# Kernel optimization log

Hardware: AMD Instinct MI355X
Metric: run time of the kernel (lower is better)

The kernel has to match this reference:

```python
import jax, jax.numpy as jnp
import numpy as np

N = 100000      # nodes
E = 3200000     # edges
F_IN = 128      # input feature dim
H = 256         # hidden dim
K = 30          # num_cluster
REG = 0.01      # regularizer coefficient


def _uniform(key, shape, fan_in):
    s = 1.0 / np.sqrt(fan_in)
    return jax.random.uniform(key, shape, jnp.float32, -s, s)


def setup_inputs() -> dict:
    key = jax.random.key(0)
    ks = jax.random.split(key, 11)
    x = jax.random.normal(ks[0], (N, F_IN), jnp.float32)
    edge_index = jax.random.randint(ks[1], (2, E), 0, N, jnp.int32)
    edge_attr = jax.random.uniform(ks[2], (E,), jnp.float32)
    return dict(
        x=x, edge_index=edge_index, edge_attr=edge_attr,
        W_conv1=_uniform(ks[3], (F_IN, H), F_IN), b_conv1=jnp.zeros((H,), jnp.float32),
        W_lin1=_uniform(ks[4], (F_IN, H), F_IN),  b_lin1=_uniform(ks[5], (H,), F_IN),
        W_conv2=_uniform(ks[6], (H, K), H),       b_conv2=jnp.zeros((K,), jnp.float32),
        W_lin2=_uniform(ks[7], (H, K), H),        b_lin2=_uniform(ks[8], (K,), H),
    )


def gcn_conv(x, W, b, row, col, w):
    """PyG GCNConv: symmetric-normalized, edge-weighted aggregation with self-loops (weight 1)."""
    n = x.shape[0]
    deg = jax.ops.segment_sum(w, col, num_segments=n) + 1.0  # self-loop weight 1
    dis = jax.lax.rsqrt(deg)                                  # deg > 0 always (self-loop)
    norm = dis[row] * w * dis[col]                            # [E]
    h = x @ W                                                 # [n, out]
    agg = jax.ops.segment_sum(norm[:, None] * h[row], col, num_segments=n)
    agg = agg + (dis * dis)[:, None] * h                      # self-loop contribution
    return agg + b


def reference(x, edge_index, edge_attr,
              W_conv1, b_conv1, W_lin1, b_lin1,
              W_conv2, b_conv2, W_lin2, b_lin2):
    row, col = edge_index[0], edge_index[1]
    # dropout is identity in eval mode
    h = jax.nn.relu(gcn_conv(x, W_conv1, b_conv1, row, col, edge_attr) + x @ W_lin1 + b_lin1)
    out = gcn_conv(h, W_conv2, b_conv2, row, col, edge_attr) + h @ W_lin2 + b_lin2
    FX = jnp.clip(jax.nn.softmax(out, axis=-1), 1e-9, 1.0 - 1e-9)  # [N, K]

    # modularity loss
    m = jnp.sum(edge_attr)
    degree = jax.ops.segment_sum(edge_attr, row, num_segments=x.shape[0])  # [N]
    connectivity = jnp.sum(edge_attr * jnp.sum(FX[row, :-1] * FX[col, :-1], axis=-1))
    s = jnp.sum(FX * degree[:, None], axis=0)[:-1]
    avg_connectivity = jnp.dot(s, s) / (2.0 * m)
    modularity = -(connectivity - avg_connectivity) / (2.0 * m)

    # collapse regularizer
    reg = (jnp.sqrt(jnp.sum(jnp.sum(FX, axis=0) ** 2) + 1e-9)
           * (FX.shape[-1] ** 0.5) / FX.shape[0] - 1.0)
    return FX, modularity + REG * reg
```

## Files before the change

kernel.cpp:

```cpp
#include <hip/hip_runtime.h>
#include <hip/hip_bf16.h>
#include <math.h>

#define N_NODES 100000
#define N_EDGES 3200000
#define F_IN 128
#define HID 256
#define KCL 30
#define NCOPY 8

typedef unsigned int uint;
typedef unsigned short ushort;
typedef unsigned char uchar;
typedef __attribute__((ext_vector_type(8))) short bf16x8;
typedef __attribute__((ext_vector_type(4))) float f32x4;
typedef __attribute__((ext_vector_type(2))) float f32x2;

static __device__ __forceinline__ float bf2f(ushort u) {
  return __uint_as_float(((uint)u) << 16);
}
static __device__ __forceinline__ ushort f2bf(float f) {
  uint u = __float_as_uint(f);
  uint r = (u + 0x7FFF + ((u >> 16) & 1)) >> 16;
  return (ushort)r;
}

static __device__ __forceinline__ uchar f2fp8(float f) {
#if __has_builtin(__builtin_amdgcn_cvt_pk_fp8_f32)
  return (uchar)(__builtin_amdgcn_cvt_pk_fp8_f32(f, f, 0, false) & 0xFF);
#else
  uint u = __float_as_uint(f);
  uint s = (u >> 24) & 0x80u;
  float a = fabsf(f);
  if (a >= 448.f) return (uchar)(s | 0x7E);
  if (a < 0.015625f) {
    int q = (int)rintf(a * 512.f);
    return (uchar)(s | (q > 8 ? 8 : q));
  }
  int e = ((int)((u >> 23) & 0xFF)) - 127;
  float step = __uint_as_float((uint)(127 + e - 3) << 23);
  int q = (int)rintf(a / step);
  if (q == 16) { e += 1; q = 8; }
  return (uchar)(s | ((e + 7) << 3) | (q - 8));
#endif
}
static __device__ __forceinline__ float fp82f_sw(uchar b) {
  uint s = ((uint)(b & 0x80u)) << 24;
  uint em = b & 0x7Fu;
  float mag;
  if ((em >> 3) == 0) mag = (float)em * 0.001953125f;
  else mag = __uint_as_float((((em >> 3) + 120) << 23) | ((em & 7u) << 20));
  return __uint_as_float(s | __float_as_uint(mag));
}
static __device__ __forceinline__ void fp8x4_dec(uint u, float* o) {
#if __has_builtin(__builtin_amdgcn_cvt_pk_f32_fp8)
  f32x2 lo = __builtin_amdgcn_cvt_pk_f32_fp8((int)u, false);
  f32x2 hi = __builtin_amdgcn_cvt_pk_f32_fp8((int)u, true);
  o[0] = lo.x; o[1] = lo.y; o[2] = hi.x; o[3] = hi.y;
#else
  o[0] = fp82f_sw(u & 0xFF); o[1] = fp82f_sw((u >> 8) & 0xFF);
  o[2] = fp82f_sw((u >> 16) & 0xFF); o[3] = fp82f_sw((u >> 24) & 0xFF);
#endif
}
static __device__ __forceinline__ float fp81_dec(uchar b) {
#if __has_builtin(__builtin_amdgcn_cvt_pk_f32_fp8)
  f32x2 lo = __builtin_amdgcn_cvt_pk_f32_fp8((int)(uint)b, false);
  return lo.x;
#else
  return fp82f_sw(b);
#endif
}
static __device__ __forceinline__ void dec29(uint4 lo, uint4 hi, float* f) {
  fp8x4_dec(lo.x, f + 0);  fp8x4_dec(lo.y, f + 4);
  fp8x4_dec(lo.z, f + 8);  fp8x4_dec(lo.w, f + 12);
  fp8x4_dec(hi.x, f + 16); fp8x4_dec(hi.y, f + 20);
  fp8x4_dec(hi.z, f + 24);
  f[28] = fp81_dec((uchar)(hi.w & 0xFF));
}


__global__ __launch_bounds__(256) void k_cnt8(const int* __restrict__ ei,
                                              int* __restrict__ cnt8) {
  int e0 = (blockIdx.x * 256 + threadIdx.x) * 4;
  int g = blockIdx.x & (NCOPY - 1);
  int4 cc = *(const int4*)(ei + N_EDGES + e0);
  int* tab = cnt8 + (size_t)g * N_NODES;
  atomicAdd(tab + cc.x, 1);
  atomicAdd(tab + cc.y, 1);
  atomicAdd(tab + cc.z, 1);
  atomicAdd(tab + cc.w, 1);
}

__global__ __launch_bounds__(1024) void k_scanA(const int* __restrict__ cnt8,
                                                int* __restrict__ off8,
                                                int* __restrict__ blocktot) {
  __shared__ int wsum[16];
  const int t = threadIdx.x;
  const int lane = t & 63, wid = t >> 6;
  int node = blockIdx.x * 1024 + t;
  int v[NCOPY];
  int tot = 0;
  if (node < N_NODES) {
    #pragma unroll
    for (int g = 0; g < NCOPY; ++g) {
      int x = cnt8[(size_t)g * N_NODES + node];
      v[g] = tot;
      tot += x;
    }
  } else {
    #pragma unroll
    for (int g = 0; g < NCOPY; ++g) v[g] = 0;
  }
  int x = tot;
  #pragma unroll
  for (int o = 1; o < 64; o <<= 1) {
    int y = __shfl_up(x, o);
    if (lane >= o) x += y;
  }
  if (lane == 63) wsum[wid] = x;
  __syncthreads();
  if (t < 16) {
    int s = wsum[t];
    #pragma unroll
    for (int o = 1; o < 16; o <<= 1) {
      int y = __shfl_up(s, o);
      if (t >= o) s += y;
    }
    wsum[t] = s;
  }
  __syncthreads();
  int excl = (wid ? wsum[wid - 1] : 0) + x - tot;
  if (node < N_NODES) {
    #pragma unroll
    for (int g = 0; g < NCOPY; ++g) off8[(size_t)node * NCOPY + g] = excl + v[g];
  }
  if (t == 0) blocktot[blockIdx.x] = wsum[15];
}

__global__ void k_scanB(const int* __restrict__ blocktot, int* __restrict__ blockoff) {
  if (threadIdx.x == 0 && blockIdx.x == 0) {
    int acc = 0;
    for (int b = 0; b < 98; ++b) { blockoff[b] = acc; acc += blocktot[b]; }
  }
}

__global__ __launch_bounds__(256) void k_scanC(int* __restrict__ off8,
                                               const int* __restrict__ blockoff) {
  int idx = blockIdx.x * 256 + threadIdx.x;
  if (idx > N_NODES * NCOPY) return;
  if (idx == N_NODES * NCOPY) { off8[idx] = N_EDGES; return; }
  off8[idx] += blockoff[idx >> 13];
}

__global__ __launch_bounds__(256) void k_csrfill8(const int* __restrict__ ei,
                                                  const float* __restrict__ w,
                                                  int* __restrict__ cnt8,
                                                  const int* __restrict__ off8,
                                                  int2* __restrict__ csr) {
  int e0 = (blockIdx.x * 256 + threadIdx.x) * 4;
  int g = blockIdx.x & (NCOPY - 1);
  int4 rr = *(const int4*)(ei + e0);
  int4 cc = *(const int4*)(ei + N_EDGES + e0);
  float4 ww = *(const float4*)(w + e0);
  int* tab = cnt8 + (size_t)g * N_NODES;
  const int rA[4] = {rr.x, rr.y, rr.z, rr.w};
  const int cA[4] = {cc.x, cc.y, cc.z, cc.w};
  const float wA[4] = {ww.x, ww.y, ww.z, ww.w};
  int idx[4];
  #pragma unroll
  for (int q = 0; q < 4; ++q) idx[q] = atomicSub(tab + cA[q], 1) - 1;
  int pos[4];
  #pragma unroll
  for (int q = 0; q < 4; ++q) pos[q] = off8[(size_t)cA[q] * NCOPY + g] + idx[q];
  #pragma unroll
  for (int q = 0; q < 4; ++q) csr[pos[q]] = make_int2(rA[q], __float_as_int(wA[q]));
}

__global__ __launch_bounds__(256) void k_degdis(const int* __restrict__ off8,
                                                const int2* __restrict__ csr,
                                                float* __restrict__ dis,
                                                float* __restrict__ m_out) {
  int n = blockIdx.x * 256 + threadIdx.x;
  float s = 0.f;
  if (n < N_NODES) {
    int e0 = off8[(size_t)n * NCOPY];
    int e1 = off8[(size_t)(n + 1) * NCOPY];
    for (int j = e0; j < e1; ++j) s += __int_as_float(csr[j].y);
    dis[n] = rsqrtf(s + 1.f);
  }
  float v = s;
  #pragma unroll
  for (int o = 32; o > 0; o >>= 1) v += __shfl_down(v, o);
  __shared__ float ls[4];
  int lane = threadIdx.x & 63, wid = threadIdx.x >> 6;
  if (lane == 0) ls[wid] = v;
  __syncthreads();
  if (threadIdx.x == 0) atomicAdd(m_out, ls[0] + ls[1] + ls[2] + ls[3]);
}

__global__ __launch_bounds__(256) void k_pn(int2* __restrict__ csr,
                                            const float* __restrict__ dis) {
  int j = blockIdx.x * 256 + threadIdx.x;
  int2 e = csr[j];
  csr[j] = make_int2(e.x, __float_as_int(__int_as_float(e.y) * dis[e.x]));
}

__global__ __launch_bounds__(256) void k_wprep(const float* __restrict__ Wc,
                                               const float* __restrict__ Wl,
                                               ushort* __restrict__ WT1) {
  int idx = blockIdx.x * 256 + threadIdx.x;
  int vc = idx >> 5;
  int kq = (idx & 31) * 4;
  const float* W = (vc < HID) ? Wc : Wl;
  int c = vc & (HID - 1);
  ushort4 u;
  u.x = f2bf(W[(size_t)(kq + 0) * HID + c]);
  u.y = f2bf(W[(size_t)(kq + 1) * HID + c]);
  u.z = f2bf(W[(size_t)(kq + 2) * HID + c]);
  u.w = f2bf(W[(size_t)(kq + 3) * HID + c]);
  *(ushort4*)(WT1 + (size_t)vc * F_IN + kq) = u;
}

__global__ __launch_bounds__(256) void k_wprep2(const float* __restrict__ Wc,
                                                const float* __restrict__ Wl,
                                                ushort* __restrict__ WT2) {
  int idx = blockIdx.x * 256 + threadIdx.x;
  int vc = idx >> 6;
  int kq = (idx & 63) * 4;
  const float* W = (vc < 32) ? Wc : Wl;
  int c = vc & 31;
  ushort4 u = make_ushort4(0, 0, 0, 0);
  if (c < KCL) {
    u.x = f2bf(W[(size_t)(kq + 0) * KCL + c]);
    u.y = f2bf(W[(size_t)(kq + 1) * KCL + c]);
    u.z = f2bf(W[(size_t)(kq + 2) * KCL + c]);
    u.w = f2bf(W[(size_t)(kq + 3) * KCL + c]);
  }
  *(ushort4*)(WT2 + (size_t)vc * HID + kq) = u;
}

__global__ __launch_bounds__(256) void k_gemm1m(const float* __restrict__ x,
                                                const ushort* __restrict__ WT1,
                                                const float* __restrict__ bc,
                                                const float* __restrict__ bl,
                                                const float* __restrict__ dis,
                                                uchar* __restrict__ hconv_f8,
                                                ushort* __restrict__ base1b) {
  __shared__ ushort xs[32 * F_IN];
  uchar* xs8 = (uchar*)xs;
  const int t = threadIdx.x;
  const int lane = t & 63, wid = t >> 6;
  const int m0 = blockIdx.x * 32;
  {
    int row = t >> 3, k0 = (t & 7) * 16;
    const float4* xp = (const float4*)(x + (size_t)(m0 + row) * F_IN + k0);
    #pragma unroll
    for (int q = 0; q < 4; ++q) {
      float4 v = xp[q];
      ushort4 u = make_ushort4(f2bf(v.x), f2bf(v.y), f2bf(v.z), f2bf(v.w));
      int k = k0 + q * 4;
      *(ushort4*)&xs[row * F_IN + (k ^ ((row & 7) << 3))] = u;
    }
  }
  __syncthreads();
  const int r0 = lane & 15, r1 = 16 + (lane & 15);
  const int kb = (lane >> 4) * 8;
  bf16x8 A0[4], A1[4];
  #pragma unroll
  for (int ks = 0; ks < 4; ++ks) {
    int k = ks * 32 + kb;
    A0[ks] = *(const bf16x8*)&xs[r0 * F_IN + (k ^ ((r0 & 7) << 3))];
    A1[ks] = *(const bf16x8*)&xs[r1 * F_IN + (k ^ ((r1 & 7) << 3))];
  }
  __syncthreads();
  const int rb = (lane >> 4) * 4;
  #pragma unroll
  for (int cb = 0; cb < 2; ++cb) {
    bf16x8 B[4][4];
    const int vbase = cb * 128 + wid * 32 + (lane & 15);
    #pragma unroll
    for (int cs = 0; cs < 2; ++cs)
      #pragma unroll
      for (int cf = 0; cf < 2; ++cf)
        #pragma unroll
        for (int ks = 0; ks < 4; ++ks) {
          int vc = cs * HID + vbase + cf * 16;
          B[cs * 2 + cf][ks] = *(const bf16x8*)(WT1 + (size_t)vc * F_IN + ks * 32 + kb);
        }
    f32x4 acc[2][4];
    #pragma unroll
    for (int fm = 0; fm < 2; ++fm)
      #pragma unroll
      for (int f = 0; f < 4; ++f) acc[fm][f] = (f32x4){0.f, 0.f, 0.f, 0.f};
    #pragma unroll
    for (int ks = 0; ks < 4; ++ks) {
      #pragma unroll
      for (int f = 0; f < 4; ++f) {
        acc[0][f] = __builtin_amdgcn_mfma_f32_16x16x32_bf16(A0[ks], B[f][ks], acc[0][f], 0, 0, 0);
        acc[1][f] = __builtin_amdgcn_mfma_f32_16x16x32_bf16(A1[ks], B[f][ks], acc[1][f], 0, 0, 0);
      }
    }
    #pragma unroll
    for (int cf = 0; cf < 2; ++cf) {
      int c = cb * 128 + wid * 32 + cf * 16 + (lane & 15);
      float bcv = bc[c], blv = bl[c];
      #pragma unroll
      for (int fm = 0; fm < 2; ++fm) {
        #pragma unroll
        for (int r = 0; r < 4; ++r) {
          int lrow = fm * 16 + rb + r;
          int row = m0 + lrow;
          float hc = acc[fm][cf][r];
          float hl = acc[fm][2 + cf][r];
          float d = dis[row];
          xs8[lrow * 256 + c] = f2fp8(hc);
          base1b[(size_t)row * HID + c] = f2bf(hl + blv + bcv + d * d * hc);
        }
      }
    }
  }
  __syncthreads();
  {
    int row = t >> 3, c0 = (t & 7) * 32;
    uint4 a = *(const uint4*)&xs8[row * 256 + c0];
    uint4 b = *(const uint4*)&xs8[row * 256 + c0 + 16];
    uchar* dst = hconv_f8 + (size_t)(m0 + row) * 256 + c0;
    *(uint4*)dst = a;
    *(uint4*)(dst + 16) = b;
  }
}

__global__ __launch_bounds__(256) void k_agg1(const int* __restrict__ off8,
                                              const int2* __restrict__ csr,
                                              const uint* __restrict__ hconv_u32,
                                              const ushort* __restrict__ base1b,
                                              const float* __restrict__ dis,
                                              ushort* __restrict__ h1b) {
  const int n = blockIdx.x;
  const int t = threadIdx.x;
  const int lane = t & 63, wid = t >> 6;
  const int e0 = off8[(size_t)n * NCOPY];
  const int e1 = off8[(size_t)(n + 1) * NCOPY];
  __shared__ int2 s_e[256];
  __shared__ float red[4][256];
  float acc0 = 0.f, acc1 = 0.f, acc2 = 0.f, acc3 = 0.f;
  for (int jb = e0; jb < e1; jb += 256) {
    int cn = min(256, e1 - jb);
    __syncthreads();
    if (t < cn) s_e[t] = csr[jb + t];
    __syncthreads();
    int j = wid;
    for (; j + 12 < cn; j += 16) {
      int2 eA = s_e[j];
      int2 eB = s_e[j + 4];
      int2 eC = s_e[j + 8];
      int2 eD = s_e[j + 12];
      uint uA = hconv_u32[(size_t)eA.x * 64 + lane];
      uint uB = hconv_u32[(size_t)eB.x * 64 + lane];
      uint uC = hconv_u32[(size_t)eC.x * 64 + lane];
      uint uD = hconv_u32[(size_t)eD.x * 64 + lane];
      float nA = __int_as_float(eA.y);
      float nB = __int_as_float(eB.y);
      float nC = __int_as_float(eC.y);
      float nD = __int_as_float(eD.y);
      float vA[4], vB[4], vC[4], vD[4];
      fp8x4_dec(uA, vA);
      fp8x4_dec(uB, vB);
      fp8x4_dec(uC, vC);
      fp8x4_dec(uD, vD);
      acc0 = fmaf(nA, vA[0], acc0); acc1 = fmaf(nA, vA[1], acc1);
      acc2 = fmaf(nA, vA[2], acc2); acc3 = fmaf(nA, vA[3], acc3);
      acc0 = fmaf(nB, vB[0], acc0); acc1 = fmaf(nB, vB[1], acc1);
      acc2 = fmaf(nB, vB[2], acc2); acc3 = fmaf(nB, vB[3], acc3);
      acc0 = fmaf(nC, vC[0], acc0); acc1 = fmaf(nC, vC[1], acc1);
      acc2 = fmaf(nC, vC[2], acc2); acc3 = fmaf(nC, vC[3], acc3);
      acc0 = fmaf(nD, vD[0], acc0); acc1 = fmaf(nD, vD[1], acc1);
      acc2 = fmaf(nD, vD[2], acc2); acc3 = fmaf(nD, vD[3], acc3);
    }
    for (; j + 4 < cn; j += 8) {
      int2 eA = s_e[j];
      int2 eB = s_e[j + 4];
      float nA = __int_as_float(eA.y);
      float nB = __int_as_float(eB.y);
      uint uA = hconv_u32[(size_t)eA.x * 64 + lane];
      uint uB = hconv_u32[(size_t)eB.x * 64 + lane];
      float vA[4], vB[4];
      fp8x4_dec(uA, vA);
      fp8x4_dec(uB, vB);
      acc0 = fmaf(nA, vA[0], acc0); acc1 = fmaf(nA, vA[1], acc1);
      acc2 = fmaf(nA, vA[2], acc2); acc3 = fmaf(nA, vA[3], acc3);
      acc0 = fmaf(nB, vB[0], acc0); acc1 = fmaf(nB, vB[1], acc1);
      acc2 = fmaf(nB, vB[2], acc2); acc3 = fmaf(nB, vB[3], acc3);
    }
    if (j < cn) {
      int2 eA = s_e[j];
      float nA = __int_as_float(eA.y);
      uint uA = hconv_u32[(size_t)eA.x * 64 + lane];
      float vA[4];
      fp8x4_dec(uA, vA);
      acc0 = fmaf(nA, vA[0], acc0); acc1 = fmaf(nA, vA[1], acc1);
      acc2 = fmaf(nA, vA[2], acc2); acc3 = fmaf(nA, vA[3], acc3);
    }
  }
  __syncthreads();
  ((float4*)red[wid])[lane] = make_float4(acc0, acc1, acc2, acc3);
  __syncthreads();
  float dn = dis[n];
  float v = dn * (red[0][t] + red[1][t] + red[2][t] + red[3][t]) + bf2f(base1b[(size_t)n * HID + t]);
  h1b[(size_t)n * HID + t] = f2bf(fmaxf(v, 0.f));
}

__global__ __launch_bounds__(256) void k_gemm2m(const ushort* __restrict__ h1b,
                                                const ushort* __restrict__ WT2,
                                                const float* __restrict__ bc,
                                                const float* __restrict__ bl,
                                                const float* __restrict__ dis,
                                                uchar* __restrict__ hconv2f8,
                                                float* __restrict__ base2p) {
  __shared__ ushort hs[64 * HID];
  const int t = threadIdx.x;
  const int lane = t & 63, wid = t >> 6;
  const int n0 = blockIdx.x * 64;
  {
    int row = t >> 2, kq = (t & 3) * 64;
    int gn = n0 + row;
    #pragma unroll
    for (int q = 0; q < 8; ++q) {
      int k = kq + q * 8;
      uint4 u = make_uint4(0, 0, 0, 0);
      if (gn < N_NODES) u = *(const uint4*)(h1b + (size_t)gn * HID + k);
      *(uint4*)&hs[row * HID + (k ^ ((row & 7) << 3))] = u;
    }
  }
  __syncthreads();
  const int lr = wid * 16 + (lane & 15);
  const int kb = (lane >> 4) * 8;
  f32x4 acc[4];
  #pragma unroll
  for (int f = 0; f < 4; ++f) acc[f] = (f32x4){0.f, 0.f, 0.f, 0.f};
  #pragma unroll
  for (int ks = 0; ks < 8; ++ks) {
    int k = ks * 32 + kb;
    bf16x8 A = *(const bf16x8*)&hs[lr * HID + (k ^ ((lr & 7) << 3))];
    #pragma unroll
    for (int f = 0; f < 4; ++f) {
      int vc = f * 16 + (lane & 15);
      bf16x8 B = *(const bf16x8*)(WT2 + (size_t)vc * HID + k);
      acc[f] = __builtin_amdgcn_mfma_f32_16x16x32_bf16(A, B, acc[f], 0, 0, 0);
    }
  }
  const int rb = (lane >> 4) * 4;
  #pragma unroll
  for (int cf = 0; cf < 2; ++cf) {
    int c = cf * 16 + (lane & 15);
    if (c < KCL) {
      float bcv = bc[c], blv = bl[c];
      #pragma unroll
      for (int r = 0; r < 4; ++r) {
        int row = n0 + wid * 16 + rb + r;
        if (row < N_NODES) {
          float hc = acc[cf][r];
          float hl = acc[2 + cf][r];
          float d = dis[row];
          hconv2f8[(size_t)row * 32 + c] = f2fp8(hc);
          base2p[(size_t)row * 32 + c] = hl + blv + bcv + d * d * hc;
        }
      }
    }
  }
}

__global__ __launch_bounds__(256) void k_agg2(const int* __restrict__ off8,
                                              const int2* __restrict__ csr,
                                              const float* __restrict__ dis,
                                              const uchar* __restrict__ hconv2f8,
                                              const float* __restrict__ base2p,
                                              float* __restrict__ FX,
                                              uchar* __restrict__ FXb8,
                                              float* __restrict__ scal) {
  const int t = threadIdx.x;
  const int lane = t & 63, wid = t >> 6;
  const int half = lane >> 5, c = lane & 31;
  const int nwaves = gridDim.x * 4;
  const int gw = blockIdx.x * 4 + wid;
  float cs_acc = 0.f;
  for (int n = gw; n < N_NODES; n += nwaves) {
    int e0 = off8[(size_t)n * NCOPY];
    int e1 = off8[(size_t)(n + 1) * NCOPY];
    float accA = 0.f, accB = 0.f;
    int j = e0 + half;
    for (; j + 2 < e1; j += 4) {
      int2 eA = csr[j];
      int2 eB = csr[j + 2];
      float p0 = __int_as_float(eA.y);
      float p1 = __int_as_float(eB.y);
      uchar b0 = hconv2f8[(size_t)eA.x * 32 + c];
      uchar b1 = hconv2f8[(size_t)eB.x * 32 + c];
      float v0 = (c < KCL) ? fp81_dec(b0) : 0.f;
      float v1 = (c < KCL) ? fp81_dec(b1) : 0.f;
      accA = fmaf(p0, v0, accA);
      accB = fmaf(p1, v1, accB);
    }
    if (j < e1) {
      int2 eA = csr[j];
      float p0 = __int_as_float(eA.y);
      uchar b0 = hconv2f8[(size_t)eA.x * 32 + c];
      float v0 = (c < KCL) ? fp81_dec(b0) : 0.f;
      accA = fmaf(p0, v0, accA);
    }
    float acc = accA + accB;
    acc += __shfl(acc, lane ^ 32);
    float out = (c < KCL) ? acc * dis[n] + base2p[(size_t)n * 32 + c] : -1e30f;
    float mx = out;
    #pragma unroll
    for (int o = 16; o > 0; o >>= 1) mx = fmaxf(mx, __shfl_xor(mx, o));
    float p = (c < KCL) ? __expf(out - mx) : 0.f;
    float sum = p;
    #pragma unroll
    for (int o = 16; o > 0; o >>= 1) sum += __shfl_xor(sum, o);
    float fx = p / sum;
    fx = fminf(fmaxf(fx, 1e-9f), 1.f - 1e-9f);
    if (half == 0 && c < KCL) {
      FX[(size_t)n * KCL + c] = fx;
      FXb8[(size_t)n * 32 + c] = f2fp8(fx);
    }
    cs_acc += (c < KCL) ? fx : 0.f;
  }
  __shared__ float red_cs[4][32];
  if (half == 0) red_cs[wid][c] = cs_acc;
  __syncthreads();
  if (t < KCL) {
    float a = red_cs[0][t] + red_cs[1][t] + red_cs[2][t] + red_cs[3][t];
    atomicAdd(&scal[2 + t], a);
  }
}

__global__ __launch_bounds__(256) void k_conn(const int* __restrict__ ei,
                                              const float* __restrict__ w,
                                              const uchar* __restrict__ FXb8,
                                              float* __restrict__ scal) {
  const int t = threadIdx.x;
  const int lane = t & 63, wid = t >> 6;
  const size_t e0 = ((size_t)blockIdx.x * 256 + t) * 4;
  float sv[29];
  #pragma unroll
  for (int k = 0; k < 29; ++k) sv[k] = 0.f;
  float conn = 0.f;
  int4 rr = *(const int4*)(ei + e0);
  int4 cc = *(const int4*)(ei + N_EDGES + e0);
  float4 ww = *(const float4*)(w + e0);
  const int rA[4] = {rr.x, rr.y, rr.z, rr.w};
  const int cA[4] = {cc.x, cc.y, cc.z, cc.w};
  const float wA[4] = {ww.x, ww.y, ww.z, ww.w};
  #pragma unroll
  for (int q = 0; q < 4; ++q) {
    int r = rA[q], cN = cA[q];
    float wv = wA[q];
    uint4 alo = *(const uint4*)(FXb8 + (size_t)r * 32);
    uint4 ahi = *(const uint4*)(FXb8 + (size_t)r * 32 + 16);
    uint4 blo = *(const uint4*)(FXb8 + (size_t)cN * 32);
    uint4 bhi = *(const uint4*)(FXb8 + (size_t)cN * 32 + 16);
    float fa[29], fb[29];
    dec29(alo, ahi, fa);
    dec29(blo, bhi, fb);
    float dot = 0.f;
    #pragma unroll
    for (int k = 0; k < 29; ++k) {
      dot += fa[k] * fb[k];
      sv[k] = fmaf(wv, fa[k], sv[k]);
    }
    conn = fmaf(wv, dot, conn);
  }
  __shared__ float red[4][30];
  #pragma unroll
  for (int i = 0; i < 30; ++i) {
    float v = (i < 29) ? sv[i] : conn;
    #pragma unroll
    for (int o = 32; o > 0; o >>= 1) v += __shfl_down(v, o);
    if (lane == 0) red[wid][i] = v;
  }
  __syncthreads();
  if (t < 30) {
    float s = red[0][t] + red[1][t] + red[2][t] + red[3][t];
    atomicAdd(t == 29 ? &scal[1] : &scal[32 + t], s);
  }
}

__global__ void k_finalize(const float* __restrict__ scal, float* __restrict__ out_loss) {
  if (threadIdx.x == 0 && blockIdx.x == 0) {
    float m = scal[0], conn = scal[1];
    float ss = 0.f;
    for (int k = 0; k < KCL - 1; ++k) { float s = scal[32 + k]; ss += s * s; }
    float cs2 = 0.f;
    for (int k = 0; k < KCL; ++k) { float cv = scal[2 + k]; cs2 += cv * cv; }
    float avg = ss / (2.f * m);
    float modularity = -(conn - avg) / (2.f * m);
    float reg = sqrtf(cs2 + 1e-9f) * sqrtf((float)KCL) / (float)N_NODES - 1.f;
    out_loss[0] = modularity + 0.01f * reg;
  }
}

extern "C" void kernel_launch(void* const* d_in, const int* in_sizes, int n_in,
                              void* d_out, int out_size, void* d_ws, size_t ws_size,
                              hipStream_t stream) {
  const float* x   = (const float*)d_in[0];
  const int*   ei  = (const int*)d_in[1];
  const float* ea  = (const float*)d_in[2];
  const float* Wc1 = (const float*)d_in[3];
  const float* bc1 = (const float*)d_in[4];
  const float* Wl1 = (const float*)d_in[5];
  const float* bl1 = (const float*)d_in[6];
  const float* Wc2 = (const float*)d_in[7];
  const float* bc2 = (const float*)d_in[8];
  const float* Wl2 = (const float*)d_in[9];
  const float* bl2 = (const float*)d_in[10];
  float* out = (float*)d_out;

  float* ws = (float*)d_ws;
  size_t o = 0;
  int*   cnt8   = (int*)(ws + o); o += (size_t)NCOPY * N_NODES;
  float* scal   = ws + o; o += 64;
  size_t zero_floats = o;
  int*   off8   = (int*)(ws + o); o += (size_t)N_NODES * NCOPY + 8;
  int*   blocktot = (int*)(ws + o); o += 128;
  int*   blockoff = (int*)(ws + o); o += 128;
  float* dis    = ws + o; o += N_NODES;
  int2*  csr    = (int2*)(ws + o); o += (size_t)N_EDGES * 2;
  ushort* WT1   = (ushort*)(ws + o); o += (size_t)512 * F_IN / 2;
  ushort* WT2   = (ushort*)(ws + o); o += (size_t)64 * HID / 2;
  uchar* hconv_f8 = (uchar*)(ws + o); o += (size_t)N_NODES * HID / 4;
  ushort* base1b = (ushort*)(ws + o); o += (size_t)N_NODES * HID / 2;
  ushort* h1b   = (ushort*)(ws + o); o += (size_t)N_NODES * HID / 2;
  uchar* hconv2f8 = (uchar*)(ws + o); o += (size_t)N_NODES * 32 / 4;
  float* base2p = ws + o; o += (size_t)N_NODES * 32;
  o += 64;
  if (ws_size < o * sizeof(float)) return;

  uchar* FXb8 = hconv_f8;

  hipMemsetAsync(d_ws, 0, zero_floats * sizeof(float), stream);

  k_cnt8<<<N_EDGES / 1024, 256, 0, stream>>>(ei, cnt8);
  k_scanA<<<98, 1024, 0, stream>>>(cnt8, off8, blocktot);
  k_scanB<<<1, 64, 0, stream>>>(blocktot, blockoff);
  k_scanC<<<(N_NODES * NCOPY + 256) / 256, 256, 0, stream>>>(off8, blockoff);
  k_csrfill8<<<N_EDGES / 1024, 256, 0, stream>>>(ei, ea, cnt8, off8, csr);
  k_degdis<<<(N_NODES + 255) / 256, 256, 0, stream>>>(off8, csr, dis, scal);
  k_pn<<<N_EDGES / 256, 256, 0, stream>>>(csr, dis);
  k_wprep<<<64, 256, 0, stream>>>(Wc1, Wl1, WT1);
  k_wprep2<<<16, 256, 0, stream>>>(Wc2, Wl2, WT2);
  k_gemm1m<<<N_NODES / 32, 256, 0, stream>>>(x, WT1, bc1, bl1, dis, hconv_f8, base1b);
  k_agg1<<<N_NODES, 256, 0, stream>>>(off8, csr, (const uint*)hconv_f8, base1b, dis, h1b);
  k_gemm2m<<<(N_NODES + 63) / 64, 256, 0, stream>>>(h1b, WT2, bc2, bl2, dis, hconv2f8, base2p);
  k_agg2<<<2048, 256, 0, stream>>>(off8, csr, dis, hconv2f8, base2p, out, FXb8, scal);
  k_conn<<<N_EDGES / 1024, 256, 0, stream>>>(ei, ea, FXb8, scal);
  k_finalize<<<1, 64, 0, stream>>>(scal, out + (size_t)N_NODES * KCL);
}
```

Before: 849.1 us.

## Compute weighted degree during counting and pre-normalize edges in CSR fill

The count kernel now also atomically accumulates per-node weighted in-degree (interleaved with counts) and the total edge weight, so a small k_dis kernel computes dis without walking the CSR. The CSR fill then writes edge weights already multiplied by dis[row], removing the separate k_degdis and k_pn passes over the 3.2M-edge CSR. In exchange there are twice as many atomics in the count kernel (a float atomic per edge), a larger interleaved table, and an extra random gather of dis during the fill. Float atomic order also makes the degree sums nondeterministic.

```diff
diff --git a/kernel.cpp b/kernel.cpp
--- a/kernel.cpp
+++ b/kernel.cpp
@@ -80,18 +80,44 @@
 
 
 __global__ __launch_bounds__(256) void k_cnt8(const int* __restrict__ ei,
-                                              int* __restrict__ cnt8) {
+                                              const float* __restrict__ w,
+                                              int* __restrict__ cd8,
+                                              float* __restrict__ m_out) {
   int e0 = (blockIdx.x * 256 + threadIdx.x) * 4;
   int g = blockIdx.x & (NCOPY - 1);
   int4 cc = *(const int4*)(ei + N_EDGES + e0);
-  int* tab = cnt8 + (size_t)g * N_NODES;
-  atomicAdd(tab + cc.x, 1);
-  atomicAdd(tab + cc.y, 1);
-  atomicAdd(tab + cc.z, 1);
-  atomicAdd(tab + cc.w, 1);
-}
-
-__global__ __launch_bounds__(1024) void k_scanA(const int* __restrict__ cnt8,
+  float4 ww = *(const float4*)(w + e0);
+  int* tab = cd8 + (size_t)g * N_NODES * 2;
+  atomicAdd(tab + (size_t)cc.x * 2, 1);
+  atomicAdd((float*)(tab + (size_t)cc.x * 2 + 1), ww.x);
+  atomicAdd(tab + (size_t)cc.y * 2, 1);
+  atomicAdd((float*)(tab + (size_t)cc.y * 2 + 1), ww.y);
+  atomicAdd(tab + (size_t)cc.z * 2, 1);
+  atomicAdd((float*)(tab + (size_t)cc.z * 2 + 1), ww.z);
+  atomicAdd(tab + (size_t)cc.w * 2, 1);
+  atomicAdd((float*)(tab + (size_t)cc.w * 2 + 1), ww.w);
+  float s = ww.x + ww.y + ww.z + ww.w;
+  #pragma unroll
+  for (int o = 32; o > 0; o >>= 1) s += __shfl_down(s, o);
+  __shared__ float ls[4];
+  int lane = threadIdx.x & 63, wid = threadIdx.x >> 6;
+  if (lane == 0) ls[wid] = s;
+  __syncthreads();
+  if (threadIdx.x == 0) atomicAdd(m_out, ls[0] + ls[1] + ls[2] + ls[3]);
+}
+
+__global__ __launch_bounds__(256) void k_dis(const int* __restrict__ cd8,
+                                             float* __restrict__ dis) {
+  int n = blockIdx.x * 256 + threadIdx.x;
+  if (n >= N_NODES) return;
+  float s = 0.f;
+  #pragma unroll
+  for (int g = 0; g < NCOPY; ++g)
+    s += __int_as_float(cd8[((size_t)g * N_NODES + n) * 2 + 1]);
+  dis[n] = rsqrtf(s + 1.f);
+}
+
+__global__ __launch_bounds__(1024) void k_scanA(const int* __restrict__ cd8,
                                                 int* __restrict__ off8,
                                                 int* __restrict__ blocktot) {
   __shared__ int wsum[16];
@@ -103,7 +129,7 @@
   if (node < N_NODES) {
     #pragma unroll
     for (int g = 0; g < NCOPY; ++g) {
-      int x = cnt8[(size_t)g * N_NODES + node];
+      int x = cd8[((size_t)g * N_NODES + node) * 2];
       v[g] = tot;
       tot += x;
     }
@@ -154,7 +180,8 @@
 
 __global__ __launch_bounds__(256) void k_csrfill8(const int* __restrict__ ei,
                                                   const float* __restrict__ w,
-                                                  int* __restrict__ cnt8,
+                                                  const float* __restrict__ dis,
+                                                  int* __restrict__ cd8,
                                                   const int* __restrict__ off8,
                                                   int2* __restrict__ csr) {
   int e0 = (blockIdx.x * 256 + threadIdx.x) * 4;
@@ -162,47 +189,21 @@
   int4 rr = *(const int4*)(ei + e0);
   int4 cc = *(const int4*)(ei + N_EDGES + e0);
   float4 ww = *(const float4*)(w + e0);
-  int* tab = cnt8 + (size_t)g * N_NODES;
+  int* tab = cd8 + (size_t)g * N_NODES * 2;
   const int rA[4] = {rr.x, rr.y, rr.z, rr.w};
   const int cA[4] = {cc.x, cc.y, cc.z, cc.w};
   const float wA[4] = {ww.x, ww.y, ww.z, ww.w};
+  float pn[4];
+  #pragma unroll
+  for (int q = 0; q < 4; ++q) pn[q] = wA[q] * dis[rA[q]];
   int idx[4];
   #pragma unroll
-  for (int q = 0; q < 4; ++q) idx[q] = atomicSub(tab + cA[q], 1) - 1;
+  for (int q = 0; q < 4; ++q) idx[q] = atomicSub(tab + (size_t)cA[q] * 2, 1) - 1;
   int pos[4];
   #pragma unroll
   for (int q = 0; q < 4; ++q) pos[q] = off8[(size_t)cA[q] * NCOPY + g] + idx[q];
   #pragma unroll
-  for (int q = 0; q < 4; ++q) csr[pos[q]] = make_int2(rA[q], __float_as_int(wA[q]));
-}
-
-__global__ __launch_bounds__(256) void k_degdis(const int* __restrict__ off8,
-                                                const int2* __restrict__ csr,
-                                                float* __restrict__ dis,
-                                                float* __restrict__ m_out) {
-  int n = blockIdx.x * 256 + threadIdx.x;
-  float s = 0.f;
-  if (n < N_NODES) {
-    int e0 = off8[(size_t)n * NCOPY];
-    int e1 = off8[(size_t)(n + 1) * NCOPY];
-    for (int j = e0; j < e1; ++j) s += __int_as_float(csr[j].y);
-    dis[n] = rsqrtf(s + 1.f);
-  }
-  float v = s;
-  #pragma unroll
-  for (int o = 32; o > 0; o >>= 1) v += __shfl_down(v, o);
-  __shared__ float ls[4];
-  int lane = threadIdx.x & 63, wid = threadIdx.x >> 6;
-  if (lane == 0) ls[wid] = v;
-  __syncthreads();
-  if (threadIdx.x == 0) atomicAdd(m_out, ls[0] + ls[1] + ls[2] + ls[3]);
-}
-
-__global__ __launch_bounds__(256) void k_pn(int2* __restrict__ csr,
-                                            const float* __restrict__ dis) {
-  int j = blockIdx.x * 256 + threadIdx.x;
-  int2 e = csr[j];
-  csr[j] = make_int2(e.x, __float_as_int(__int_as_float(e.y) * dis[e.x]));
+  for (int q = 0; q < 4; ++q) csr[pos[q]] = make_int2(rA[q], __float_as_int(pn[q]));
 }
 
 __global__ __launch_bounds__(256) void k_wprep(const float* __restrict__ Wc,
@@ -618,7 +619,7 @@
 
   float* ws = (float*)d_ws;
   size_t o = 0;
-  int*   cnt8   = (int*)(ws + o); o += (size_t)NCOPY * N_NODES;
+  int*   cd8    = (int*)(ws + o); o += (size_t)NCOPY * N_NODES * 2;
   float* scal   = ws + o; o += 64;
   size_t zero_floats = o;
   int*   off8   = (int*)(ws + o); o += (size_t)N_NODES * NCOPY + 8;
@@ -640,13 +641,12 @@
 
   hipMemsetAsync(d_ws, 0, zero_floats * sizeof(float), stream);
 
-  k_cnt8<<<N_EDGES / 1024, 256, 0, stream>>>(ei, cnt8);
-  k_scanA<<<98, 1024, 0, stream>>>(cnt8, off8, blocktot);
+  k_cnt8<<<N_EDGES / 1024, 256, 0, stream>>>(ei, ea, cd8, scal);
+  k_scanA<<<98, 1024, 0, stream>>>(cd8, off8, blocktot);
   k_scanB<<<1, 64, 0, stream>>>(blocktot, blockoff);
   k_scanC<<<(N_NODES * NCOPY + 256) / 256, 256, 0, stream>>>(off8, blockoff);
-  k_csrfill8<<<N_EDGES / 1024, 256, 0, stream>>>(ei, ea, cnt8, off8, csr);
-  k_degdis<<<(N_NODES + 255) / 256, 256, 0, stream>>>(off8, csr, dis, scal);
-  k_pn<<<N_EDGES / 256, 256, 0, stream>>>(csr, dis);
+  k_dis<<<(N_NODES + 255) / 256, 256, 0, stream>>>(cd8, dis);
+  k_csrfill8<<<N_EDGES / 1024, 256, 0, stream>>>(ei, ea, dis, cd8, off8, csr);
   k_wprep<<<64, 256, 0, stream>>>(Wc1, Wl1, WT1);
   k_wprep2<<<16, 256, 0, stream>>>(Wc2, Wl2, WT2);
   k_gemm1m<<<N_NODES / 32, 256, 0, stream>>>(x, WT1, bc1, bl1, dis, hconv_f8, base1b);
```

After: 1.008 ms. 18.7% more time.
